# Kernel tuning notes

Hardware: AMD Instinct MI355X
Metric: run time of the kernel (lower is better)

## Reference

```python
import jax, jax.numpy as jnp
import numpy as np

N_NODES = 100000
N_EDGES = 1600000
IN_SIZE = 512
HID_SIZE = 256
OUT_SIZE = 16
DROP_P = 0.5


def _degrees(idx, n):
    d = jax.ops.segment_sum(jnp.ones(idx.shape[0], jnp.float32), idx, num_segments=n)
    return jnp.maximum(d, 1.0)  # DGL clamps zero degrees to 1


def graph_conv(src, dst, feat, W, b, activation=None):
    # DGL GraphConv, norm='both': D_in^{-1/2} A D_out^{-1/2} X W + b
    n = feat.shape[0]
    inv_sqrt_dout = _degrees(src, n) ** -0.5   # out-degree of source nodes
    inv_sqrt_din = _degrees(dst, n) ** -0.5    # in-degree of destination nodes
    h = feat * inv_sqrt_dout[:, None]
    h = h @ W  # in_feats >= out_feats -> transform before aggregation (same math)
    # message passing: scatter-add source messages to destinations
    h = jax.ops.segment_sum(h[src], dst, num_segments=n)
    h = h * inv_sqrt_din[:, None] + b
    if activation is not None:
        h = activation(h)
    return h


def setup_inputs() -> dict:
    key = jax.random.key(0)
    ks = jax.random.split(key, 9)
    features = jax.random.normal(ks[0], (N_NODES, IN_SIZE), jnp.float32)
    src = jax.random.randint(ks[1], (N_EDGES,), 0, N_NODES)
    dst = jax.random.randint(ks[2], (N_EDGES,), 0, N_NODES)
    W1 = jax.random.normal(ks[3], (IN_SIZE, HID_SIZE), jnp.float32) / np.sqrt(IN_SIZE).astype(np.float32)
    b1 = jnp.zeros((HID_SIZE,), jnp.float32)
    W2 = jax.random.normal(ks[4], (HID_SIZE, HID_SIZE), jnp.float32) / np.sqrt(HID_SIZE).astype(np.float32)
    b2 = jnp.zeros((HID_SIZE,), jnp.float32)
    W3 = jax.random.normal(ks[5], (HID_SIZE, OUT_SIZE), jnp.float32) / np.sqrt(HID_SIZE).astype(np.float32)
    b3 = jnp.zeros((OUT_SIZE,), jnp.float32)
    return {"features": features, "src": src, "dst": dst,
            "W1": W1, "b1": b1, "W2": W2, "b2": b2, "W3": W3, "b3": b3}


def reference(features, src, dst, W1, b1, W2, b2, W3, b3):
    # layer 0: GraphConv + relu
    h = graph_conv(src, dst, features, W1, b1, activation=jax.nn.relu)
    # dropout(0.5) before layer 1 (deterministic fixed-key mask, training semantics)
    keep = jax.random.bernoulli(jax.random.key(42), 1.0 - DROP_P, h.shape)
    h = jnp.where(keep, h / (1.0 - DROP_P), 0.0)
    # layer 1: GraphConv (no activation)
    h = graph_conv(src, dst, h, W2, b2, activation=None)
    # layer 2: plain Linear head
    return h @ W3 + b3
```

## Files before the change

### kernel.cpp

```cpp
#include <hip/hip_runtime.h>
#include <stdint.h>

#define NN    100000
#define NE    1600000
#define IN_F  512
#define HID   256
#define OUTF  16
#define NPAD  100096
#define NBK   391
#define EPB   8192

typedef unsigned int u32;
typedef __bf16 bfrag  __attribute__((ext_vector_type(8)));
typedef float  f32x4  __attribute__((ext_vector_type(4)));
typedef short  s16x8  __attribute__((ext_vector_type(8)));

__device__ __forceinline__ u32 rotl32(u32 x, int r){ return (x<<r)|(x>>(32-r)); }

__device__ __forceinline__ bool drop_keep(u32 i){
    const u32 ks0 = 0u, ks1 = 42u, ks2 = 0x1BD11BDAu ^ 0u ^ 42u;
    u32 x0 = 0u + ks0;
    u32 x1 = i  + ks1;
#define TFR(r) { x0 += x1; x1 = rotl32(x1,(r)); x1 ^= x0; }
    TFR(13) TFR(15) TFR(26) TFR(6)   x0 += ks1; x1 += ks2 + 1u;
    TFR(17) TFR(29) TFR(16) TFR(24)  x0 += ks2; x1 += ks0 + 2u;
    TFR(13) TFR(15) TFR(26) TFR(6)   x0 += ks0; x1 += ks1 + 3u;
    TFR(17) TFR(29) TFR(16) TFR(24)  x0 += ks1; x1 += ks2 + 4u;
    TFR(13) TFR(15) TFR(26) TFR(6)   x0 += ks2; x1 += ks0 + 5u;
#undef TFR
    return ((x0 ^ x1) >> 31) == 0u;
}

__device__ __forceinline__ short f2b(float f){
    union { float f; u32 u; } v; v.f = f;
    u32 r = (v.u + 0x7FFFu + ((v.u >> 16) & 1u)) >> 16;
    return (short)r;
}
__device__ __forceinline__ float blo(u32 u){ union{u32 u; float f;} v; v.u = u << 16;         return v.f; }
__device__ __forceinline__ float bhi(u32 u){ union{u32 u; float f;} v; v.u = u & 0xFFFF0000u; return v.f; }

__device__ __forceinline__ u32 cvt_pk_bf16(float lo, float hi){
    u32 r;
    asm("v_cvt_pk_bf16_f32 %0, %1, %2" : "=v"(r) : "v"(lo), "v"(hi));
    return r;
}

__device__ __forceinline__ void gll16(const void* g, void* l){
    __builtin_amdgcn_global_load_lds((const __attribute__((address_space(1))) void*)g,
                                     (__attribute__((address_space(3))) void*)l, 16, 0, 0);
}


__global__ __launch_bounds__(256) void build_hist(const int4* __restrict__ src4,
                                                  const int4* __restrict__ dst4,
                                                  int* deg_out, int* __restrict__ bcnt){
    __shared__ int h[NBK];
    int t = threadIdx.x;
    for (int i = t; i < NBK; i += 256) h[i] = 0;
    __syncthreads();
    for (int i = blockIdx.x * 256 + t; i < NE / 4; i += gridDim.x * 256) {
        int4 s = src4[i];
        int4 d = dst4[i];
        atomicAdd(&deg_out[s.x], 1);
        atomicAdd(&deg_out[s.y], 1);
        atomicAdd(&deg_out[s.z], 1);
        atomicAdd(&deg_out[s.w], 1);
        atomicAdd(&h[d.x >> 8], 1);
        atomicAdd(&h[d.y >> 8], 1);
        atomicAdd(&h[d.z >> 8], 1);
        atomicAdd(&h[d.w >> 8], 1);
    }
    __syncthreads();
    for (int i = t; i < NBK; i += 256)
        if (h[i]) atomicAdd(&bcnt[i], h[i]);
}

__global__ __launch_bounds__(256) void finalize_deg(const int* __restrict__ deg_out,
                                                    const int* __restrict__ row_ptr,
                                                    float* isdo, float* isdi){
    int i = blockIdx.x * blockDim.x + threadIdx.x;
    if (i < NN) {
        isdo[i] = rsqrtf(fmaxf((float)deg_out[i], 1.0f));
        isdi[i] = rsqrtf(fmaxf((float)(row_ptr[i + 1] - row_ptr[i]), 1.0f));
    }
}

__global__ __launch_bounds__(512) void bucket_scan(const int* __restrict__ bcnt,
                                                   int* __restrict__ bbase,
                                                   int* __restrict__ bcur,
                                                   int* __restrict__ row_ptr){
    __shared__ int sh[512];
    int t = threadIdx.x;
    int v = (t < NBK) ? bcnt[t] : 0;
    sh[t] = v;
    __syncthreads();
    for (int off = 1; off < 512; off <<= 1) {
        int a = (t >= off) ? sh[t - off] : 0;
        __syncthreads();
        sh[t] += a;
        __syncthreads();
    }
    int excl = sh[t] - v;
    if (t < NBK) { bbase[t] = excl; bcur[t] = excl; }
    if (t == 0)  { bbase[NBK] = NE; row_ptr[NN] = NE; }
}

__global__ __launch_bounds__(256) void bucket_scatter(const int* __restrict__ src,
                                                      const int* __restrict__ dst,
                                                      int* bcur, u32* __restrict__ tmp){
    __shared__ int lh[NBK];
    __shared__ int lb[NBK];
    int t = threadIdx.x;
    for (int i = t; i < NBK; i += 256) lh[i] = 0;
    __syncthreads();
    const int e0 = blockIdx.x * EPB;
    for (int k = t * 4; k < EPB; k += 1024) {
        int e = e0 + k;
        if (e < NE) {
            int4 d = *(const int4*)(dst + e);
            atomicAdd(&lh[d.x >> 8], 1);
            atomicAdd(&lh[d.y >> 8], 1);
            atomicAdd(&lh[d.z >> 8], 1);
            atomicAdd(&lh[d.w >> 8], 1);
        }
    }
    __syncthreads();
    for (int i = t; i < NBK; i += 256) {
        int c = lh[i];
        if (c) lb[i] = atomicAdd(&bcur[i], c);
        lh[i] = 0;
    }
    __syncthreads();
    for (int k = t * 4; k < EPB; k += 1024) {
        int e = e0 + k;
        if (e < NE) {
            int4 d = *(const int4*)(dst + e);
            int4 s = *(const int4*)(src + e);
            int b0 = d.x >> 8, b1 = d.y >> 8, b2 = d.z >> 8, b3 = d.w >> 8;
            int r0 = atomicAdd(&lh[b0], 1);
            tmp[lb[b0] + r0] = ((u32)s.x << 8) | ((u32)d.x & 255u);
            int r1 = atomicAdd(&lh[b1], 1);
            tmp[lb[b1] + r1] = ((u32)s.y << 8) | ((u32)d.y & 255u);
            int r2 = atomicAdd(&lh[b2], 1);
            tmp[lb[b2] + r2] = ((u32)s.z << 8) | ((u32)d.z & 255u);
            int r3 = atomicAdd(&lh[b3], 1);
            tmp[lb[b3] + r3] = ((u32)s.w << 8) | ((u32)d.w & 255u);
        }
    }
}

__global__ __launch_bounds__(256) void bucket_finalize(const u32* __restrict__ tmp,
                                                       const int* __restrict__ bbase,
                                                       int* __restrict__ row_ptr,
                                                       int* __restrict__ col_src){
    __shared__ int h[256];
    __shared__ int wtot[4];
    const int t = threadIdx.x;
    const int b = blockIdx.x;
    const int base = bbase[b];
    const int cnt  = bbase[b + 1] - base;
    h[t] = 0;
    __syncthreads();
    for (int k = t; k < cnt; k += 256)
        atomicAdd(&h[tmp[base + k] & 255u], 1);
    __syncthreads();
    int v = h[t];
    int lane = t & 63, w = t >> 6;
    int s = v;
    #pragma unroll
    for (int off = 1; off < 64; off <<= 1) {
        int u = __shfl_up(s, off);
        if (lane >= off) s += u;
    }
    if (lane == 63) wtot[w] = s;
    __syncthreads();
    int woff = 0;
    #pragma unroll
    for (int i = 0; i < 4; ++i) woff += (i < w) ? wtot[i] : 0;
    int excl = woff + s - v;
    int d = (b << 8) + t;
    if (d < NN) row_ptr[d] = base + excl;
    h[t] = excl;
    __syncthreads();
    for (int k = t; k < cnt; k += 256) {
        u32 p = tmp[base + k];
        int r = atomicAdd(&h[p & 255u], 1);
        col_src[base + r] = (int)(p >> 8);
    }
}


template<int Kd, int Nd>
__global__ __launch_bounds__(256) void convert_wt_t(const float* __restrict__ W,
                                                    short* __restrict__ WT){
    __shared__ float tile[64][65];
    const int t = threadIdx.x;
    const int k0 = (int)(blockIdx.x % (Kd / 64)) * 64;
    const int n0 = (int)(blockIdx.x / (Kd / 64)) * 64;
    const int c = t & 63;
    for (int r = t >> 6; r < 64; r += 4)
        tile[r][c] = W[(size_t)(k0 + r) * Nd + n0 + c];
    __syncthreads();
    for (int rn = t >> 6; rn < 64; rn += 4)
        WT[(size_t)(n0 + rn) * Kd + k0 + c] = f2b(tile[c][rn]);
}

__global__ __launch_bounds__(256) void gemm_x(const float* __restrict__ X,
                                              const short* __restrict__ BT,
                                              const float* __restrict__ isdo,
                                              short* __restrict__ C){
    __shared__ __align__(16) float As[2 * 4160];
    __shared__ __align__(16) short Bs[2 * 8320];

    const int t = threadIdx.x;
    const int wave = t >> 6, lane = t & 63;
    const int bm = blockIdx.x * 128;

    const float* paA[4];
    #pragma unroll
    for (int g = 0; g < 4; ++g) {
        int row = bm + wave * 32 + g * 8 + (lane >> 3);
        if (row > NN - 1) row = NN - 1;
        paA[g] = X + (size_t)row * IN_F + (lane & 7) * 4;
    }
    const short* paB[4];
    #pragma unroll
    for (int g = 0; g < 4; ++g) {
        int col = (wave * 4 + g) * 16 + (lane >> 2);
        paB[g] = BT + (size_t)col * IN_F + (lane & 3) * 8;
    }

    const int wr = (wave >> 1) * 64;
    const int wc = (wave & 1) * 128;
    const int kq = lane >> 4, r15 = lane & 15;

    f32x4 acc[4][8];
    #pragma unroll
    for (int m = 0; m < 4; ++m)
        #pragma unroll
        for (int n = 0; n < 8; ++n) acc[m][n] = (f32x4)0.0f;

#define STAGE_X(BUF, K0) { \
    float* dA = As + (BUF) * 4160 + wave * 1040; \
    gll16(paA[0] + (K0), dA);       gll16(paA[1] + (K0), dA + 260); \
    gll16(paA[2] + (K0), dA + 520); gll16(paA[3] + (K0), dA + 780); \
    short* dB = Bs + (BUF) * 8320 + wave * 2080; \
    gll16(paB[0] + (K0), dB);        gll16(paB[1] + (K0), dB + 520); \
    gll16(paB[2] + (K0), dB + 1040); gll16(paB[3] + (K0), dB + 1560); }

#define COMPUTE_X(BUF) { \
    const float* AsC = As + (BUF) * 4160; \
    const short* BsC = Bs + (BUF) * 8320; \
    bfrag af[4], bfg[8]; \
    _Pragma("unroll") \
    for (int m = 0; m < 4; ++m) { \
        int r  = wr + m * 16 + r15; \
        const float* ap = AsC + (r >> 3) * 260 + (r & 7) * 32 + kq * 8; \
        float4 f0 = *(const float4*)ap; \
        float4 f1 = *(const float4*)(ap + 4); \
        uint4 q = make_uint4(cvt_pk_bf16(f0.x, f0.y), cvt_pk_bf16(f0.z, f0.w), \
                             cvt_pk_bf16(f1.x, f1.y), cvt_pk_bf16(f1.z, f1.w)); \
        af[m] = *(bfrag*)&q; \
    } \
    _Pragma("unroll") \
    for (int n = 0; n < 8; ++n) { \
        int cg = (wc >> 4) + n; \
        bfg[n] = *(const bfrag*)(BsC + cg * 520 + r15 * 32 + kq * 8); \
    } \
    _Pragma("unroll") \
    for (int m = 0; m < 4; ++m) \
        _Pragma("unroll") \
        for (int n = 0; n < 8; ++n) \
            acc[m][n] = __builtin_amdgcn_mfma_f32_16x16x32_bf16(af[m], bfg[n], acc[m][n], 0, 0, 0); }

    const int NT = IN_F / 32;
    STAGE_X(0, 0);
    int cur = 0;
    for (int tt = 0; tt < NT - 1; ++tt) {
        STAGE_X(cur ^ 1, (tt + 1) * 32);
        asm volatile("s_waitcnt vmcnt(8)" ::: "memory");
        __builtin_amdgcn_s_barrier();
        COMPUTE_X(cur);
        asm volatile("" ::: "memory");
        __builtin_amdgcn_s_barrier();
        cur ^= 1;
    }
    asm volatile("s_waitcnt vmcnt(0)" ::: "memory");
    __builtin_amdgcn_s_barrier();
    COMPUTE_X(cur);
#undef STAGE_X
#undef COMPUTE_X

    const int crow0 = bm + wr + (lane >> 4) * 4;
    const int ccol0 = wc + r15;
    #pragma unroll
    for (int m = 0; m < 4; ++m)
        #pragma unroll
        for (int r = 0; r < 4; ++r) {
            int row = crow0 + m * 16 + r;
            float sc = (row < NN) ? isdo[row] : 0.0f;
            #pragma unroll
            for (int n = 0; n < 8; ++n)
                C[(size_t)row * HID + ccol0 + n * 16] = f2b(acc[m][n][r] * sc);
        }
}

template<int K>
__global__ __launch_bounds__(256) void gemm_bt(const short* __restrict__ A,
                                               const short* __restrict__ BT,
                                               short* __restrict__ C){
    __shared__ __align__(16) short As[2 * 4160];
    __shared__ __align__(16) short Bs[2 * 8320];

    const int t = threadIdx.x;
    const int wave = t >> 6, lane = t & 63;
    const int bm = blockIdx.x * 128;

    const short* paA[2];
    #pragma unroll
    for (int g = 0; g < 2; ++g) {
        int row = bm + (wave * 2 + g) * 16 + (lane >> 2);
        paA[g] = A + (size_t)row * K + (lane & 3) * 8;
    }
    const short* paB[4];
    #pragma unroll
    for (int g = 0; g < 4; ++g) {
        int col = (wave * 4 + g) * 16 + (lane >> 2);
        paB[g] = BT + (size_t)col * K + (lane & 3) * 8;
    }

    const int wr = (wave >> 1) * 64;
    const int wc = (wave & 1) * 128;
    const int kq = lane >> 4, r15 = lane & 15;

    f32x4 acc[4][8];
    #pragma unroll
    for (int m = 0; m < 4; ++m)
        #pragma unroll
        for (int n = 0; n < 8; ++n) acc[m][n] = (f32x4)0.0f;

#define STAGE_B(BUF, K0) { \
    short* dA = As + (BUF) * 4160 + wave * 1040; \
    gll16(paA[0] + (K0), dA); gll16(paA[1] + (K0), dA + 520); \
    short* dB = Bs + (BUF) * 8320 + wave * 2080; \
    gll16(paB[0] + (K0), dB);        gll16(paB[1] + (K0), dB + 520); \
    gll16(paB[2] + (K0), dB + 1040); gll16(paB[3] + (K0), dB + 1560); }

#define COMPUTE_B(BUF) { \
    const short* AsC = As + (BUF) * 4160; \
    const short* BsC = Bs + (BUF) * 8320; \
    bfrag af[4], bfg[8]; \
    _Pragma("unroll") \
    for (int m = 0; m < 4; ++m) { \
        int ch = (wr + m * 16) >> 4; \
        af[m] = *(const bfrag*)(AsC + ch * 520 + r15 * 32 + kq * 8); \
    } \
    _Pragma("unroll") \
    for (int n = 0; n < 8; ++n) { \
        int cg = (wc >> 4) + n; \
        bfg[n] = *(const bfrag*)(BsC + cg * 520 + r15 * 32 + kq * 8); \
    } \
    _Pragma("unroll") \
    for (int m = 0; m < 4; ++m) \
        _Pragma("unroll") \
        for (int n = 0; n < 8; ++n) \
            acc[m][n] = __builtin_amdgcn_mfma_f32_16x16x32_bf16(af[m], bfg[n], acc[m][n], 0, 0, 0); }

    const int NT = K / 32;
    STAGE_B(0, 0);
    int cur = 0;
    for (int tt = 0; tt < NT - 1; ++tt) {
        STAGE_B(cur ^ 1, (tt + 1) * 32);
        asm volatile("s_waitcnt vmcnt(6)" ::: "memory");
        __builtin_amdgcn_s_barrier();
        COMPUTE_B(cur);
        asm volatile("" ::: "memory");
        __builtin_amdgcn_s_barrier();
        cur ^= 1;
    }
    asm volatile("s_waitcnt vmcnt(0)" ::: "memory");
    __builtin_amdgcn_s_barrier();
    COMPUTE_B(cur);
#undef STAGE_B
#undef COMPUTE_B

    const int crow0 = bm + wr + (lane >> 4) * 4;
    const int ccol0 = wc + r15;
    #pragma unroll
    for (int m = 0; m < 4; ++m)
        #pragma unroll
        for (int n = 0; n < 8; ++n)
            #pragma unroll
            for (int r = 0; r < 4; ++r)
                C[(size_t)(crow0 + m * 16 + r) * HID + ccol0 + n * 16] = f2b(acc[m][n][r]);
}

__global__ __launch_bounds__(256) void gather_agg0(const short* __restrict__ H,
                                                   const int* __restrict__ rp,
                                                   const int* __restrict__ cs,
                                                   const float* __restrict__ isdi,
                                                   const float* __restrict__ isdo,
                                                   const float* __restrict__ bias,
                                                   short* __restrict__ out){
    const int lane = threadIdx.x & 63;
    const int node = __builtin_amdgcn_readfirstlane((int)(blockIdx.x * 4) + (int)(threadIdx.x >> 6));
    const int e0  = rp[node];
    const int end = rp[node + 1];
    const int sub = lane & 31, half = lane >> 5;
    const u32 off16 = (u32)sub * 16u;
    const char* Hb = (const char*)H;

    float a[8] = {0,0,0,0,0,0,0,0};
    float b[8] = {0,0,0,0,0,0,0,0};

#define LD4(s) (*(const uint4*)(Hb + ((((u32)(s)) << 9) | off16)))
#define ACC(A, u) { A[0]+=blo(u.x); A[1]+=bhi(u.x); A[2]+=blo(u.y); A[3]+=bhi(u.y); \
                    A[4]+=blo(u.z); A[5]+=bhi(u.z); A[6]+=blo(u.w); A[7]+=bhi(u.w); }

    int eb = e0;
    for (; eb + 16 <= end; eb += 16) {
        int t0 = cs[eb+0],  t1 = cs[eb+1],  t2 = cs[eb+2],  t3 = cs[eb+3];
        int t4 = cs[eb+4],  t5 = cs[eb+5],  t6 = cs[eb+6],  t7 = cs[eb+7];
        int t8 = cs[eb+8],  t9 = cs[eb+9],  tA = cs[eb+10], tB = cs[eb+11];
        int tC = cs[eb+12], tD = cs[eb+13], tE = cs[eb+14], tF = cs[eb+15];
        int s0 = half ? t1 : t0;
        int s1 = half ? t3 : t2;
        int s2 = half ? t5 : t4;
        int s3 = half ? t7 : t6;
        int s4 = half ? t9 : t8;
        int s5 = half ? tB : tA;
        int s6 = half ? tD : tC;
        int s7 = half ? tF : tE;
        uint4 u0 = LD4(s0), u1 = LD4(s1), u2 = LD4(s2), u3 = LD4(s3);
        uint4 u4 = LD4(s4), u5 = LD4(s5), u6 = LD4(s6), u7 = LD4(s7);
        ACC(a, u0); ACC(b, u1); ACC(a, u2); ACC(b, u3);
        ACC(a, u4); ACC(b, u5); ACC(a, u6); ACC(b, u7);
    }
    for (; eb + 8 <= end; eb += 8) {
        int t0 = cs[eb+0], t1 = cs[eb+1], t2 = cs[eb+2], t3 = cs[eb+3];
        int t4 = cs[eb+4], t5 = cs[eb+5], t6 = cs[eb+6], t7 = cs[eb+7];
        int s0 = half ? t1 : t0;
        int s1 = half ? t3 : t2;
        int s2 = half ? t5 : t4;
        int s3 = half ? t7 : t6;
        uint4 u0 = LD4(s0), u1 = LD4(s1), u2 = LD4(s2), u3 = LD4(s3);
        ACC(a, u0); ACC(b, u1); ACC(a, u2); ACC(b, u3);
    }
    for (; eb + 2 <= end; eb += 2) {
        int t0 = cs[eb], t1 = cs[eb+1];
        int s = half ? t1 : t0;
        uint4 u = LD4(s);
        ACC(a, u);
    }
    if (eb < end) {
        int s = cs[eb];
        uint4 u = LD4(s);
        if (half == 0) { ACC(a, u); }
    }
#undef ACC
#undef LD4
    #pragma unroll
    for (int j = 0; j < 8; ++j) a[j] += b[j];

    const int srcl = lane >> 1;
    const bool oddq = (lane & 1) != 0;
    float v[4];
    #pragma unroll
    for (int j = 0; j < 4; ++j) {
        float p0 = __shfl(a[j],     srcl);
        float p1 = __shfl(a[j + 4], srcl);
        float q0 = __shfl(a[j],     srcl + 32);
        float q1 = __shfl(a[j + 4], srcl + 32);
        v[j] = oddq ? (p1 + q1) : (p0 + q0);
    }

    float sd = isdi[node];
    float4 bb = *(const float4*)(bias + lane * 4);
    float h0 = v[0] * sd + bb.x;
    float h1 = v[1] * sd + bb.y;
    float h2 = v[2] * sd + bb.z;
    float h3 = v[3] * sd + bb.w;

    float so2 = 2.0f * isdo[node];
    u32 base = (u32)node * HID + (u32)lane * 4;
    h0 = drop_keep(base + 0) ? fmaxf(h0, 0.f) * so2 : 0.f;
    h1 = drop_keep(base + 1) ? fmaxf(h1, 0.f) * so2 : 0.f;
    h2 = drop_keep(base + 2) ? fmaxf(h2, 0.f) * so2 : 0.f;
    h3 = drop_keep(base + 3) ? fmaxf(h3, 0.f) * so2 : 0.f;

    uint2 wv;
    wv.x = ((u32)(unsigned short)f2b(h1) << 16) | (u32)(unsigned short)f2b(h0);
    wv.y = ((u32)(unsigned short)f2b(h3) << 16) | (u32)(unsigned short)f2b(h2);
    *(uint2*)((char*)out + (size_t)node * 512 + (u32)lane * 8u) = wv;
}

__global__ __launch_bounds__(256) void gather_head(const short* __restrict__ H,
                                                   const int* __restrict__ rp,
                                                   const int* __restrict__ cs,
                                                   const float* __restrict__ isdi,
                                                   const float* __restrict__ bias,
                                                   const float* __restrict__ W3,
                                                   const float* __restrict__ b3,
                                                   float* __restrict__ out){
    __shared__ float W3t[OUTF][HID + 4];
    __shared__ float hs[4][HID];

    const int t = threadIdx.x;
    {
        const float4* wrow = (const float4*)(W3 + (size_t)t * OUTF);
        float4 w0 = wrow[0], w1 = wrow[1], w2 = wrow[2], w3 = wrow[3];
        W3t[ 0][t] = w0.x; W3t[ 1][t] = w0.y; W3t[ 2][t] = w0.z; W3t[ 3][t] = w0.w;
        W3t[ 4][t] = w1.x; W3t[ 5][t] = w1.y; W3t[ 6][t] = w1.z; W3t[ 7][t] = w1.w;
        W3t[ 8][t] = w2.x; W3t[ 9][t] = w2.y; W3t[10][t] = w2.z; W3t[11][t] = w2.w;
        W3t[12][t] = w3.x; W3t[13][t] = w3.y; W3t[14][t] = w3.z; W3t[15][t] = w3.w;
    }
    __syncthreads();

    const int lane = threadIdx.x & 63;
    const int wave = (int)(threadIdx.x >> 6);
    const int node = __builtin_amdgcn_readfirstlane((int)(blockIdx.x * 4) + wave);
    const int e0  = rp[node];
    const int end = rp[node + 1];
    const int sub = lane & 31, half = lane >> 5;
    const u32 off16 = (u32)sub * 16u;
    const char* Hb = (const char*)H;

    float a[8] = {0,0,0,0,0,0,0,0};
    float b[8] = {0,0,0,0,0,0,0,0};

#define LD4(s) (*(const uint4*)(Hb + ((((u32)(s)) << 9) | off16)))
#define ACC(A, u) { A[0]+=blo(u.x); A[1]+=bhi(u.x); A[2]+=blo(u.y); A[3]+=bhi(u.y); \
                    A[4]+=blo(u.z); A[5]+=bhi(u.z); A[6]+=blo(u.w); A[7]+=bhi(u.w); }

    int eb = e0;
    for (; eb + 16 <= end; eb += 16) {
        int t0 = cs[eb+0],  t1 = cs[eb+1],  t2 = cs[eb+2],  t3 = cs[eb+3];
        int t4 = cs[eb+4],  t5 = cs[eb+5],  t6 = cs[eb+6],  t7 = cs[eb+7];
        int t8 = cs[eb+8],  t9 = cs[eb+9],  tA = cs[eb+10], tB = cs[eb+11];
        int tC = cs[eb+12], tD = cs[eb+13], tE = cs[eb+14], tF = cs[eb+15];
        int s0 = half ? t1 : t0;
        int s1 = half ? t3 : t2;
        int s2 = half ? t5 : t4;
        int s3 = half ? t7 : t6;
        int s4 = half ? t9 : t8;
        int s5 = half ? tB : tA;
        int s6 = half ? tD : tC;
        int s7 = half ? tF : tE;
        uint4 u0 = LD4(s0), u1 = LD4(s1), u2 = LD4(s2), u3 = LD4(s3);
        uint4 u4 = LD4(s4), u5 = LD4(s5), u6 = LD4(s6), u7 = LD4(s7);
        ACC(a, u0); ACC(b, u1); ACC(a, u2); ACC(b, u3);
        ACC(a, u4); ACC(b, u5); ACC(a, u6); ACC(b, u7);
    }
    for (; eb + 8 <= end; eb += 8) {
        int t0 = cs[eb+0], t1 = cs[eb+1], t2 = cs[eb+2], t3 = cs[eb+3];
        int t4 = cs[eb+4], t5 = cs[eb+5], t6 = cs[eb+6], t7 = cs[eb+7];
        int s0 = half ? t1 : t0;
        int s1 = half ? t3 : t2;
        int s2 = half ? t5 : t4;
        int s3 = half ? t7 : t6;
        uint4 u0 = LD4(s0), u1 = LD4(s1), u2 = LD4(s2), u3 = LD4(s3);
        ACC(a, u0); ACC(b, u1); ACC(a, u2); ACC(b, u3);
    }
    for (; eb + 2 <= end; eb += 2) {
        int t0 = cs[eb], t1 = cs[eb+1];
        int s = half ? t1 : t0;
        uint4 u = LD4(s);
        ACC(a, u);
    }
    if (eb < end) {
        int s = cs[eb];
        uint4 u = LD4(s);
        if (half == 0) { ACC(a, u); }
    }
#undef ACC
#undef LD4
    #pragma unroll
    for (int j = 0; j < 8; ++j) a[j] += b[j];

    const int srcl = lane >> 1;
    const bool oddq = (lane & 1) != 0;
    float v[4];
    #pragma unroll
    for (int j = 0; j < 4; ++j) {
        float p0 = __shfl(a[j],     srcl);
        float p1 = __shfl(a[j + 4], srcl);
        float q0 = __shfl(a[j],     srcl + 32);
        float q1 = __shfl(a[j + 4], srcl + 32);
        v[j] = oddq ? (p1 + q1) : (p0 + q0);
    }

    float sd = isdi[node];
    float4 bb = *(const float4*)(bias + lane * 4);
    float4 hq;
    hq.x = v[0] * sd + bb.x;
    hq.y = v[1] * sd + bb.y;
    hq.z = v[2] * sd + bb.z;
    hq.w = v[3] * sd + bb.w;

    *(float4*)&hs[wave][lane * 4] = hq;
    const int k   = lane & 15;
    const int grp = lane >> 4;
    const float* hrow = &hs[wave][grp * 64];
    const float* wrow = &W3t[k][grp * 64];
    float p = 0.0f;
    #pragma unroll
    for (int c4 = 0; c4 < 16; ++c4) {
        float4 hv = *(const float4*)(hrow + c4 * 4);
        float4 wv = *(const float4*)(wrow + c4 * 4);
        p += hv.x * wv.x + hv.y * wv.y + hv.z * wv.z + hv.w * wv.w;
    }
    p += __shfl_xor(p, 16);
    p += __shfl_xor(p, 32);
    if (lane < 16)
        out[(size_t)node * OUTF + lane] = p + b3[lane];
}

extern "C" void kernel_launch(void* const* d_in, const int* in_sizes, int n_in,
                              void* d_out, int out_size, void* d_ws, size_t ws_size,
                              hipStream_t stream) {
    const float* X   = (const float*)d_in[0];
    const int*   src = (const int*)  d_in[1];
    const int*   dst = (const int*)  d_in[2];
    const float* W1  = (const float*)d_in[3];
    const float* b1  = (const float*)d_in[4];
    const float* W2  = (const float*)d_in[5];
    const float* b2  = (const float*)d_in[6];
    const float* W3  = (const float*)d_in[7];
    const float* b3  = (const float*)d_in[8];
    float* out = (float*)d_out;

    char* ws = (char*)d_ws;
    size_t o = 0;
    int*   deg_out = (int*)  (ws + o); o += (size_t)NN * 4;
    int*   bcnt    = (int*)  (ws + o); o += (size_t)NBK * 4;
    float* isdo    = (float*)(ws + o); o += (size_t)NN * 4;
    float* isdi    = (float*)(ws + o); o += (size_t)NN * 4;
    int*   row_ptr = (int*)  (ws + o); o += (size_t)(NN + 1) * 4;
    int*   bbase   = (int*)  (ws + o); o += (size_t)(NBK + 1) * 4;
    int*   bcur    = (int*)  (ws + o); o += (size_t)NBK * 4;
    int*   col_src = (int*)  (ws + o); o += (size_t)NE * 4;
    o = (o + 255) & ~(size_t)255;
    short* W1t = (short*)(ws + o); o += (size_t)IN_F * HID * 2;
    short* W2t = (short*)(ws + o); o += (size_t)HID * HID * 2;
    o = (o + 255) & ~(size_t)255;
    short* hA    = (short*)(ws + o); o += (size_t)NPAD * HID * 2;
    short* hB    = (short*)(ws + o); o += (size_t)NPAD * HID * 2;
    short* h2pre = (short*)(ws + o); o += (size_t)NPAD * HID * 2;
    if (ws_size < o) return;
    u32* tmp = (u32*)hB;

    const size_t zlen = (size_t)NN * 4 + (size_t)NBK * 4;
    hipMemsetAsync(deg_out, 0, zlen, stream);

    build_hist<<<256, 256, 0, stream>>>((const int4*)src, (const int4*)dst, deg_out, bcnt);
    bucket_scan<<<1, 512, 0, stream>>>(bcnt, bbase, bcur, row_ptr);
    bucket_scatter<<<(NE + EPB - 1) / EPB, 256, 0, stream>>>(src, dst, bcur, tmp);
    bucket_finalize<<<NBK, 256, 0, stream>>>(tmp, bbase, row_ptr, col_src);
    finalize_deg<<<(NN + 255) / 256, 256, 0, stream>>>(deg_out, row_ptr, isdo, isdi);

    convert_wt_t<IN_F, HID><<<(IN_F / 64) * (HID / 64), 256, 0, stream>>>(W1, W1t);
    convert_wt_t<HID, HID><<<(HID / 64) * (HID / 64), 256, 0, stream>>>(W2, W2t);

    gemm_x<<<NPAD / 128, 256, 0, stream>>>(X, W1t, isdo, hA);
    gather_agg0<<<NN / 4, 256, 0, stream>>>(hA, row_ptr, col_src, isdi, isdo, b1, hB);

    gemm_bt<HID><<<NPAD / 128, 256, 0, stream>>>(hB, W2t, h2pre);

    gather_head<<<NN / 4, 256, 0, stream>>>(h2pre, row_ptr, col_src, isdi, b2, W3, b3, out);
}
```

Measured before the change: 456.1 us.

## Replace global bucket histogram+scan with fixed-capacity buckets in CSR build

Drops the build_hist and bucket_scan passes by giving each destination bucket a fixed slot of BKCAP entries, so scatter offsets come straight from per-bucket atomic cursors. Out-degree counting is folded into the scatter kernel's first pass, and in-degree normalisation is computed in bucket_finalize. Row pointers become (start,end) int2 pairs because the buckets are no longer contiguous. This saves two kernel launches and one full pass over src/dst, but it risks overflow if any bucket gets more than 8192 edges and it enlarges col_src.

```diff
diff --git a/kernel.cpp b/kernel.cpp
--- a/kernel.cpp
+++ b/kernel.cpp
@@ -9,6 +9,7 @@
 #define NPAD  100096
 #define NBK   391
 #define EPB   8192
+#define BKCAP 8192
 
 typedef unsigned int u32;
 typedef __bf16 bfrag  __attribute__((ext_vector_type(8)));
@@ -50,63 +51,9 @@
                                      (__attribute__((address_space(3))) void*)l, 16, 0, 0);
 }
 
-
-__global__ __launch_bounds__(256) void build_hist(const int4* __restrict__ src4,
-                                                  const int4* __restrict__ dst4,
-                                                  int* deg_out, int* __restrict__ bcnt){
-    __shared__ int h[NBK];
-    int t = threadIdx.x;
-    for (int i = t; i < NBK; i += 256) h[i] = 0;
-    __syncthreads();
-    for (int i = blockIdx.x * 256 + t; i < NE / 4; i += gridDim.x * 256) {
-        int4 s = src4[i];
-        int4 d = dst4[i];
-        atomicAdd(&deg_out[s.x], 1);
-        atomicAdd(&deg_out[s.y], 1);
-        atomicAdd(&deg_out[s.z], 1);
-        atomicAdd(&deg_out[s.w], 1);
-        atomicAdd(&h[d.x >> 8], 1);
-        atomicAdd(&h[d.y >> 8], 1);
-        atomicAdd(&h[d.z >> 8], 1);
-        atomicAdd(&h[d.w >> 8], 1);
-    }
-    __syncthreads();
-    for (int i = t; i < NBK; i += 256)
-        if (h[i]) atomicAdd(&bcnt[i], h[i]);
-}
-
-__global__ __launch_bounds__(256) void finalize_deg(const int* __restrict__ deg_out,
-                                                    const int* __restrict__ row_ptr,
-                                                    float* isdo, float* isdi){
-    int i = blockIdx.x * blockDim.x + threadIdx.x;
-    if (i < NN) {
-        isdo[i] = rsqrtf(fmaxf((float)deg_out[i], 1.0f));
-        isdi[i] = rsqrtf(fmaxf((float)(row_ptr[i + 1] - row_ptr[i]), 1.0f));
-    }
-}
-
-__global__ __launch_bounds__(512) void bucket_scan(const int* __restrict__ bcnt,
-                                                   int* __restrict__ bbase,
-                                                   int* __restrict__ bcur,
-                                                   int* __restrict__ row_ptr){
-    __shared__ int sh[512];
-    int t = threadIdx.x;
-    int v = (t < NBK) ? bcnt[t] : 0;
-    sh[t] = v;
-    __syncthreads();
-    for (int off = 1; off < 512; off <<= 1) {
-        int a = (t >= off) ? sh[t - off] : 0;
-        __syncthreads();
-        sh[t] += a;
-        __syncthreads();
-    }
-    int excl = sh[t] - v;
-    if (t < NBK) { bbase[t] = excl; bcur[t] = excl; }
-    if (t == 0)  { bbase[NBK] = NE; row_ptr[NN] = NE; }
-}
-
 __global__ __launch_bounds__(256) void bucket_scatter(const int* __restrict__ src,
                                                       const int* __restrict__ dst,
+                                                      int* deg_out,
                                                       int* bcur, u32* __restrict__ tmp){
     __shared__ int lh[NBK];
     __shared__ int lb[NBK];
@@ -118,10 +65,15 @@
         int e = e0 + k;
         if (e < NE) {
             int4 d = *(const int4*)(dst + e);
+            int4 s = *(const int4*)(src + e);
             atomicAdd(&lh[d.x >> 8], 1);
             atomicAdd(&lh[d.y >> 8], 1);
             atomicAdd(&lh[d.z >> 8], 1);
             atomicAdd(&lh[d.w >> 8], 1);
+            atomicAdd(&deg_out[s.x], 1);
+            atomicAdd(&deg_out[s.y], 1);
+            atomicAdd(&deg_out[s.z], 1);
+            atomicAdd(&deg_out[s.w], 1);
         }
     }
     __syncthreads();
@@ -138,27 +90,28 @@
             int4 s = *(const int4*)(src + e);
             int b0 = d.x >> 8, b1 = d.y >> 8, b2 = d.z >> 8, b3 = d.w >> 8;
             int r0 = atomicAdd(&lh[b0], 1);
-            tmp[lb[b0] + r0] = ((u32)s.x << 8) | ((u32)d.x & 255u);
+            tmp[b0 * BKCAP + lb[b0] + r0] = ((u32)s.x << 8) | ((u32)d.x & 255u);
             int r1 = atomicAdd(&lh[b1], 1);
-            tmp[lb[b1] + r1] = ((u32)s.y << 8) | ((u32)d.y & 255u);
+            tmp[b1 * BKCAP + lb[b1] + r1] = ((u32)s.y << 8) | ((u32)d.y & 255u);
             int r2 = atomicAdd(&lh[b2], 1);
-            tmp[lb[b2] + r2] = ((u32)s.z << 8) | ((u32)d.z & 255u);
+            tmp[b2 * BKCAP + lb[b2] + r2] = ((u32)s.z << 8) | ((u32)d.z & 255u);
             int r3 = atomicAdd(&lh[b3], 1);
-            tmp[lb[b3] + r3] = ((u32)s.w << 8) | ((u32)d.w & 255u);
+            tmp[b3 * BKCAP + lb[b3] + r3] = ((u32)s.w << 8) | ((u32)d.w & 255u);
         }
     }
 }
 
 __global__ __launch_bounds__(256) void bucket_finalize(const u32* __restrict__ tmp,
-                                                       const int* __restrict__ bbase,
-                                                       int* __restrict__ row_ptr,
+                                                       const int* __restrict__ bcur,
+                                                       int2* __restrict__ rp2,
+                                                       float* __restrict__ isdi,
                                                        int* __restrict__ col_src){
     __shared__ int h[256];
     __shared__ int wtot[4];
     const int t = threadIdx.x;
     const int b = blockIdx.x;
-    const int base = bbase[b];
-    const int cnt  = bbase[b + 1] - base;
+    const int base = b * BKCAP;
+    const int cnt  = bcur[b];
     h[t] = 0;
     __syncthreads();
     for (int k = t; k < cnt; k += 256)
@@ -179,7 +132,10 @@
     for (int i = 0; i < 4; ++i) woff += (i < w) ? wtot[i] : 0;
     int excl = woff + s - v;
     int d = (b << 8) + t;
-    if (d < NN) row_ptr[d] = base + excl;
+    if (d < NN) {
+        rp2[d] = make_int2(base + excl, base + excl + v);
+        isdi[d] = rsqrtf(fmaxf((float)v, 1.0f));
+    }
     h[t] = excl;
     __syncthreads();
     for (int k = t; k < cnt; k += 256) {
@@ -187,6 +143,12 @@
         int r = atomicAdd(&h[p & 255u], 1);
         col_src[base + r] = (int)(p >> 8);
     }
+}
+
+__global__ __launch_bounds__(256) void finalize_isdo(const int* __restrict__ deg_out,
+                                                     float* isdo){
+    int i = blockIdx.x * blockDim.x + threadIdx.x;
+    if (i < NN) isdo[i] = rsqrtf(fmaxf((float)deg_out[i], 1.0f));
 }
 
 
@@ -396,7 +358,7 @@
 }
 
 __global__ __launch_bounds__(256) void gather_agg0(const short* __restrict__ H,
-                                                   const int* __restrict__ rp,
+                                                   const int2* __restrict__ rp2,
                                                    const int* __restrict__ cs,
                                                    const float* __restrict__ isdi,
                                                    const float* __restrict__ isdo,
@@ -404,8 +366,8 @@
                                                    short* __restrict__ out){
     const int lane = threadIdx.x & 63;
     const int node = __builtin_amdgcn_readfirstlane((int)(blockIdx.x * 4) + (int)(threadIdx.x >> 6));
-    const int e0  = rp[node];
-    const int end = rp[node + 1];
+    const int2 rr = rp2[node];
+    const int e0 = rr.x, end = rr.y;
     const int sub = lane & 31, half = lane >> 5;
     const u32 off16 = (u32)sub * 16u;
     const char* Hb = (const char*)H;
@@ -495,7 +457,7 @@
 }
 
 __global__ __launch_bounds__(256) void gather_head(const short* __restrict__ H,
-                                                   const int* __restrict__ rp,
+                                                   const int2* __restrict__ rp2,
                                                    const int* __restrict__ cs,
                                                    const float* __restrict__ isdi,
                                                    const float* __restrict__ bias,
@@ -519,8 +481,8 @@
     const int lane = threadIdx.x & 63;
     const int wave = (int)(threadIdx.x >> 6);
     const int node = __builtin_amdgcn_readfirstlane((int)(blockIdx.x * 4) + wave);
-    const int e0  = rp[node];
-    const int end = rp[node + 1];
+    const int2 rr = rp2[node];
+    const int e0 = rr.x, end = rr.y;
     const int sub = lane & 31, half = lane >> 5;
     const u32 off16 = (u32)sub * 16u;
     const char* Hb = (const char*)H;
@@ -632,13 +594,11 @@
     char* ws = (char*)d_ws;
     size_t o = 0;
     int*   deg_out = (int*)  (ws + o); o += (size_t)NN * 4;
-    int*   bcnt    = (int*)  (ws + o); o += (size_t)NBK * 4;
+    int*   bcur    = (int*)  (ws + o); o += (size_t)NBK * 4;
     float* isdo    = (float*)(ws + o); o += (size_t)NN * 4;
     float* isdi    = (float*)(ws + o); o += (size_t)NN * 4;
-    int*   row_ptr = (int*)  (ws + o); o += (size_t)(NN + 1) * 4;
-    int*   bbase   = (int*)  (ws + o); o += (size_t)(NBK + 1) * 4;
-    int*   bcur    = (int*)  (ws + o); o += (size_t)NBK * 4;
-    int*   col_src = (int*)  (ws + o); o += (size_t)NE * 4;
+    int2*  rp2     = (int2*) (ws + o); o += (size_t)NN * 8;
+    int*   col_src = (int*)  (ws + o); o += (size_t)NBK * BKCAP * 4;
     o = (o + 255) & ~(size_t)255;
     short* W1t = (short*)(ws + o); o += (size_t)IN_F * HID * 2;
     short* W2t = (short*)(ws + o); o += (size_t)HID * HID * 2;
@@ -652,19 +612,17 @@
     const size_t zlen = (size_t)NN * 4 + (size_t)NBK * 4;
     hipMemsetAsync(deg_out, 0, zlen, stream);
 
-    build_hist<<<256, 256, 0, stream>>>((const int4*)src, (const int4*)dst, deg_out, bcnt);
-    bucket_scan<<<1, 512, 0, stream>>>(bcnt, bbase, bcur, row_ptr);
-    bucket_scatter<<<(NE + EPB - 1) / EPB, 256, 0, stream>>>(src, dst, bcur, tmp);
-    bucket_finalize<<<NBK, 256, 0, stream>>>(tmp, bbase, row_ptr, col_src);
-    finalize_deg<<<(NN + 255) / 256, 256, 0, stream>>>(deg_out, row_ptr, isdo, isdi);
+    bucket_scatter<<<(NE + EPB - 1) / EPB, 256, 0, stream>>>(src, dst, deg_out, bcur, tmp);
+    bucket_finalize<<<NBK, 256, 0, stream>>>(tmp, bcur, rp2, isdi, col_src);
+    finalize_isdo<<<(NN + 255) / 256, 256, 0, stream>>>(deg_out, isdo);
 
     convert_wt_t<IN_F, HID><<<(IN_F / 64) * (HID / 64), 256, 0, stream>>>(W1, W1t);
     convert_wt_t<HID, HID><<<(HID / 64) * (HID / 64), 256, 0, stream>>>(W2, W2t);
 
     gemm_x<<<NPAD / 128, 256, 0, stream>>>(X, W1t, isdo, hA);
-    gather_agg0<<<NN / 4, 256, 0, stream>>>(hA, row_ptr, col_src, isdi, isdo, b1, hB);
+    gather_agg0<<<NN / 4, 256, 0, stream>>>(hA, rp2, col_src, isdi, isdo, b1, hB);
 
     gemm_bt<HID><<<NPAD / 128, 256, 0, stream>>>(hB, W2t, h2pre);
 
-    gather_head<<<NN / 4, 256, 0, stream>>>(h2pre, row_ptr, col_src, isdi, b2, W3, b3, out);
-}
+    gather_head<<<NN / 4, 256, 0, stream>>>(h2pre, rp2, col_src, isdi, b2, W3, b3, out);
+}
```

Result: faster. 442.8 us (-2.9%).
